# Kernel optimization log

Measured on AMD Instinct MI355X. Metric: run time of the kernel, lower is better.

## Reference

```python
import jax, jax.numpy as jnp
import numpy as np

N, E, B = 50000, 400000, 8
ND, ED, H, L = 32, 16, 128, 3

def setup_inputs() -> dict:
    key = jax.random.key(0)
    ks = jax.random.split(key, 32)
    s = 0.05
    inp = {
        'x': jax.random.normal(ks[0], (N, ND), jnp.float32),
        'edge_attr': jax.random.normal(ks[1], (E, ED), jnp.float32),
        'global_feature': jax.random.normal(ks[2], (B, 1), jnp.float32),
        'edge_index': jax.random.randint(ks[3], (2, E), 0, N, jnp.int64),
        'batch': jnp.sort(jax.random.randint(ks[4], (N,), 0, B, jnp.int64)),
        # embeddings
        'Wn': jax.random.normal(ks[5], (ND, H), jnp.float32) * s,
        'bn': jnp.zeros((H,), jnp.float32),
        'We': jax.random.normal(ks[6], (ED, H), jnp.float32) * s,
        'be': jnp.zeros((H,), jnp.float32),
        'Wg': jax.random.normal(ks[7], (1, H), jnp.float32) * s,
        'bg': jnp.zeros((H,), jnp.float32),
        # message-passing layers (stacked over L)
        'mW1': jax.random.normal(ks[8], (L, 3 * H, H), jnp.float32) * s,
        'mb1': jnp.zeros((L, H), jnp.float32),
        'mW2': jax.random.normal(ks[9], (L, H, H), jnp.float32) * s,
        'mb2': jnp.zeros((L, H), jnp.float32),
        'uW1': jax.random.normal(ks[10], (L, 2 * H, H), jnp.float32) * s,
        'ub1': jnp.zeros((L, H), jnp.float32),
        'uW2': jax.random.normal(ks[11], (L, H, H), jnp.float32) * s,
        'ub2': jnp.zeros((L, H), jnp.float32),
        # readout MLP
        'rW1': jax.random.normal(ks[12], (2 * H, H), jnp.float32) * s,
        'rb1': jnp.zeros((H,), jnp.float32),
        'rW2': jax.random.normal(ks[13], (H, H // 2), jnp.float32) * s,
        'rb2': jnp.zeros((H // 2,), jnp.float32),
        'rW3': jax.random.normal(ks[14], (H // 2, 1), jnp.float32) * s,
        'rb3': jnp.zeros((1,), jnp.float32),
    }
    return inp

def reference(x, edge_attr, global_feature, Wn, bn, We, be, Wg, bg,
              mW1, mb1, mW2, mb2, uW1, ub1, uW2, ub2,
              rW1, rb1, rW2, rb2, rW3, rb3, edge_index, batch):
    h = x @ Wn + bn                      # [N,H]
    e = edge_attr @ We + be              # [E,H]
    g = global_feature @ Wg + bg         # [B,H]
    src, dst = edge_index[0], edge_index[1]  # PyG: x_j=source, x_i=target, aggregate at target
    for l in range(L):
        m_in = jnp.concatenate([h[dst], h[src], e], axis=1)            # [E,3H]
        m = jax.nn.relu(m_in @ mW1[l] + mb1[l]) @ mW2[l] + mb2[l]       # [E,H]
        aggr = jax.ops.segment_sum(m, dst, num_segments=N)              # [N,H]
        u_in = jnp.concatenate([h, aggr], axis=1)                       # [N,2H]
        upd = jax.nn.relu(u_in @ uW1[l] + ub1[l]) @ uW2[l] + ub2[l]
        h = h + upd
    counts = jax.ops.segment_sum(jnp.ones((N,), h.dtype), batch, num_segments=B)
    pooled = jax.ops.segment_sum(h, batch, num_segments=B) / jnp.maximum(counts, 1.0)[:, None]
    final = jnp.concatenate([pooled, g], axis=1)                        # [B,2H]
    out = jax.nn.relu(final @ rW1 + rb1)
    out = jax.nn.relu(out @ rW2 + rb2)
    return out @ rW3 + rb3                                              # [B,1]
```

## Files before the change

### kernel.cpp

```cpp
#include <hip/hip_runtime.h>

#define NN 50000
#define NPAD 50048
#define NE 400000
#define NBATCH 8
#define NDIM 32
#define EDIM 16
#define H 128
#define NLAYERS 3
#define CHUNK_ELEMS 4096
#define NODE_CHUNKS 24
#define ZW_CHUNK 8192
#define NSB 196
#define ZEB 128

#define EMB_B 1563
#define DEG_B 1563
#define ZWB (NLAYERS * 8)
#define WEFB NLAYERS
#define WUB (NLAYERS * 257)
#define P1_B (EMB_B + DEG_B + ZWB + WEFB + WUB)
#define K2_B (NSB + NLAYERS * NODE_CHUNKS)
#define ZDZS_B (NPAD / 64)
#define ZE_B (NE / ZEB)
#define ZZ_B (ZDZS_B + ZE_B)

typedef __attribute__((ext_vector_type(8))) __bf16 bf16x8;
typedef __attribute__((ext_vector_type(16))) float f32x16;
typedef __attribute__((ext_vector_type(8))) short short8;
typedef __attribute__((ext_vector_type(2))) float v2f;

__device__ __forceinline__ void block_sync_lds() {
  asm volatile("s_waitcnt lgkmcnt(0)\ns_barrier" ::: "memory");
}
__device__ __forceinline__ v2f bf2f(unsigned u) {
  v2f r;
  r.x = __uint_as_float(u << 16);
  r.y = __uint_as_float(u & 0xffff0000u);
  return r;
}

__global__ __launch_bounds__(256) void p1_kernel(
    const float* __restrict__ x, const float* __restrict__ Wn,
    const float* __restrict__ bn, __bf16* __restrict__ hb,
    const int* __restrict__ ei, int* __restrict__ deg,
    const float* __restrict__ mW1, __bf16* __restrict__ ZW,
    const float* __restrict__ mb1, const float* __restrict__ We,
    const float* __restrict__ be, __bf16* __restrict__ WefS,
    float* __restrict__ bm, const float* __restrict__ uW1,
    const float* __restrict__ mW2, const float* __restrict__ mb2,
    float* __restrict__ Wu, float* __restrict__ va) {
  __shared__ __align__(16) float smem[NDIM * H + 32 * NDIM];
  int bi = blockIdx.x;
  int tid = threadIdx.x;
  if (bi < EMB_B) {
    float* Ws = smem;
    float* xs = smem + NDIM * H;
    int nbase = bi * 32;
    for (int f = tid; f < NDIM * H; f += 256) Ws[f] = Wn[f];
    for (int f = tid; f < 32 * NDIM; f += 256) {
      int gi = nbase * NDIM + f;
      xs[f] = (gi < NN * NDIM) ? x[gi] : 0.f;
    }
    __syncthreads();
    int j = tid & 127, g = tid >> 7;
    float wcol[NDIM];
#pragma unroll
    for (int k = 0; k < NDIM; ++k) wcol[k] = Ws[k * H + j];
    float b = bn[j];
    for (int nn = 0; nn < 16; ++nn) {
      int node = nbase + g * 16 + nn;
      if (node < NN) {
        float acc = b;
        const float4* xv = (const float4*)&xs[(g * 16 + nn) * NDIM];
#pragma unroll
        for (int k4 = 0; k4 < NDIM / 4; ++k4) {
          float4 v = xv[k4];
          acc = fmaf(v.x, wcol[k4 * 4 + 0], acc);
          acc = fmaf(v.y, wcol[k4 * 4 + 1], acc);
          acc = fmaf(v.z, wcol[k4 * 4 + 2], acc);
          acc = fmaf(v.w, wcol[k4 * 4 + 3], acc);
        }
        hb[(size_t)node * H + j] = (__bf16)acc;
      }
    }
  } else if (bi < EMB_B + DEG_B) {
    int e = (bi - EMB_B) * 256 + tid;
    if (e < NE) atomicAdd(&deg[ei[NE + e]], 1);
  } else if (bi < EMB_B + DEG_B + ZWB) {
    int bb = bi - EMB_B - DEG_B;
    int l = bb / 8;
    int c = bb % 8;
    const float* w1 = mW1 + (size_t)l * 384 * H;
    __bf16* dst = ZW + ((size_t)l * 8 + c) * ZW_CHUNK;
    for (int it = 0; it < 32; it += 4) {
      float wv[4];
#pragma unroll
      for (int q = 0; q < 4; ++q) {
        int flat = (it + q) * 256 + tid;
        int j = flat & 7;
        int lane = (flat >> 3) & 63;
        int nt = (flat >> 9) & 7;
        int k = c * 16 + ((lane >> 5) << 3) + j;
        int n = nt * 32 + (lane & 31);
        wv[q] = (n < 128) ? w1[(size_t)k * H + n]
                          : w1[(size_t)(128 + k) * H + (n - 128)];
      }
#pragma unroll
      for (int q = 0; q < 4; ++q) {
        int flat = (it + q) * 256 + tid;
        int hilo = flat >> 12;
        __bf16 hi = (__bf16)wv[q];
        __bf16 lo = (__bf16)(wv[q] - (float)hi);
        dst[flat] = hilo ? lo : hi;
      }
    }
  } else if (bi < EMB_B + DEG_B + ZWB + WEFB) {
    int l = bi - (EMB_B + DEG_B + ZWB);
    float* WeS = smem;
    float* beS = smem + 2048;
    float* wefT = smem + 2176;
    for (int f = tid; f < EDIM * H; f += 256) WeS[f] = We[f];
    if (tid < 128) beS[tid] = be[tid];
    __syncthreads();
    if (tid < 128) {
      int n = tid;
      const float* w1 = mW1 + (size_t)l * 384 * H + (size_t)256 * H + n;
      float acc[EDIM];
#pragma unroll
      for (int i = 0; i < EDIM; ++i) acc[i] = 0.f;
      float accb = 0.f;
      for (int c = 0; c < H; c += 4) {
        float w0 = w1[(size_t)(c + 0) * H];
        float w1v = w1[(size_t)(c + 1) * H];
        float w2 = w1[(size_t)(c + 2) * H];
        float w3 = w1[(size_t)(c + 3) * H];
        accb = fmaf(beS[c + 0], w0, accb);
        accb = fmaf(beS[c + 1], w1v, accb);
        accb = fmaf(beS[c + 2], w2, accb);
        accb = fmaf(beS[c + 3], w3, accb);
#pragma unroll
        for (int i = 0; i < EDIM; ++i) {
          acc[i] = fmaf(WeS[i * H + c + 0], w0, acc[i]);
          acc[i] = fmaf(WeS[i * H + c + 1], w1v, acc[i]);
          acc[i] = fmaf(WeS[i * H + c + 2], w2, acc[i]);
          acc[i] = fmaf(WeS[i * H + c + 3], w3, acc[i]);
        }
      }
#pragma unroll
      for (int i = 0; i < EDIM; ++i) wefT[i * H + n] = acc[i];
      bm[l * H + n] = mb1[l * H + n] + accb;
    }
    __syncthreads();
    {
      int nt = tid >> 6, lane = tid & 63;
      int n = nt * 32 + (lane & 31);
      int half = lane >> 5;
      __bf16* dst = WefS + (size_t)l * CHUNK_ELEMS;
#pragma unroll
      for (int j = 0; j < 8; ++j) {
        int k = half * 8 + j;
        float w = wefT[k * H + n];
        __bf16 hi = (__bf16)w;
        __bf16 lo = (__bf16)(w - (float)hi);
        dst[((0 * 4 + nt) * 64 + lane) * 8 + j] = hi;
        dst[((1 * 4 + nt) * 64 + lane) * 8 + j] = lo;
      }
    }
  } else {
    int bb = bi - (EMB_B + DEG_B + ZWB + WEFB);
    int l = bb / 257;
    int r = bb % 257;
    int j = tid & 127, hf = tid >> 7;
    const float* u1 = uW1 + (size_t)l * 256 * H;
    if (r < 128) {
      if (tid < 128) Wu[((size_t)l * 256 + r) * H + j] = u1[(size_t)r * H + j];
    } else {
      float* rowS = smem;
      float* redS = smem + 128;
      if (tid < 128)
        rowS[tid] = (r < 256) ? mW2[((size_t)l * H + (r - 128)) * H + tid]
                              : mb2[l * H + tid];
      __syncthreads();
      int cb = hf * 64;
      float s0 = 0.f, s1 = 0.f, s2 = 0.f, s3 = 0.f;
      for (int c = 0; c < 64; c += 4) {
        float a0 = u1[(size_t)(128 + cb + c + 0) * H + j];
        float a1 = u1[(size_t)(128 + cb + c + 1) * H + j];
        float a2 = u1[(size_t)(128 + cb + c + 2) * H + j];
        float a3 = u1[(size_t)(128 + cb + c + 3) * H + j];
        s0 = fmaf(rowS[cb + c + 0], a0, s0);
        s1 = fmaf(rowS[cb + c + 1], a1, s1);
        s2 = fmaf(rowS[cb + c + 2], a2, s2);
        s3 = fmaf(rowS[cb + c + 3], a3, s3);
      }
      float s = (s0 + s1) + (s2 + s3);
      if (hf == 1) redS[j] = s;
      __syncthreads();
      if (hf == 0) {
        float tot = s + redS[j];
        if (r < 256) Wu[((size_t)l * 256 + r) * H + j] = tot;
        else va[l * H + j] = tot;
      }
    }
  }
}

__global__ __launch_bounds__(256) void k2_kernel(
    const int* __restrict__ deg, int* __restrict__ bsum,
    const float* __restrict__ Wu, const float* __restrict__ uW2,
    __bf16* __restrict__ WnS) {
  __shared__ int ws[4];
  int bi = blockIdx.x;
  int tid = threadIdx.x;
  if (bi < NSB) {
    int i = bi * 256 + tid;
    int lane = tid & 63, wid = tid >> 6;
    int v = (i < NN) ? deg[i] : 0;
#pragma unroll
    for (int off = 32; off; off >>= 1) v += __shfl_down(v, off);
    if (lane == 0) ws[wid] = v;
    __syncthreads();
    if (tid == 0) bsum[bi] = ws[0] + ws[1] + ws[2] + ws[3];
  } else {
    int idx = bi - NSB;
    int l = idx / NODE_CHUNKS;
    int c = idx % NODE_CHUNKS;
    int nt = tid >> 6, lane = tid & 63;
    int n = nt * 32 + (lane & 31);
    int half = lane >> 5;
    __bf16* dst = WnS + ((size_t)l * NODE_CHUNKS + c) * CHUNK_ELEMS;
#pragma unroll
    for (int j = 0; j < 8; ++j) {
      float w;
      if (c < 16) {
        int k = c * 16 + half * 8 + j;
        w = Wu[((size_t)l * 256 + k) * H + n];
      } else {
        int k = (c - 16) * 16 + half * 8 + j;
        w = uW2[((size_t)l * H + k) * H + n];
      }
      __bf16 hi = (__bf16)w;
      __bf16 lo = (__bf16)(w - (float)hi);
      dst[((0 * 4 + nt) * 64 + lane) * 8 + j] = hi;
      dst[((1 * 4 + nt) * 64 + lane) * 8 + j] = lo;
    }
  }
}

__global__ __launch_bounds__(256) void scan2_kernel(const int* __restrict__ bsum,
                                                    int* __restrict__ boff) {
  __shared__ int s[256];
  int t = threadIdx.x;
  int v = (t < NSB) ? bsum[t] : 0;
  s[t] = v;
  __syncthreads();
  for (int off = 1; off < 256; off <<= 1) {
    int u = (t >= off) ? s[t - off] : 0;
    __syncthreads();
    s[t] += u;
    __syncthreads();
  }
  if (t < NSB) boff[t] = s[t] - v;
}

__global__ __launch_bounds__(256) void scan3_kernel(const int* __restrict__ deg,
                                                    const int* __restrict__ boff,
                                                    int* __restrict__ cursor) {
  __shared__ int wsum[4], woff[4];
  int i = blockIdx.x * 256 + threadIdx.x;
  int lane = threadIdx.x & 63, wid = threadIdx.x >> 6;
  int orig = (i < NN) ? deg[i] : 0;
  int v = orig;
#pragma unroll
  for (int off = 1; off < 64; off <<= 1) {
    int u = __shfl_up(v, off);
    if (lane >= off) v += u;
  }
  if (lane == 63) wsum[wid] = v;
  __syncthreads();
  if (threadIdx.x == 0) {
    int r = 0;
#pragma unroll
    for (int w = 0; w < 4; ++w) {
      woff[w] = r;
      r += wsum[w];
    }
  }
  __syncthreads();
  if (i < NN) cursor[i] = (v - orig) + woff[wid] + boff[blockIdx.x];
}

__global__ __launch_bounds__(256) void scatter_kernel(
    const int* __restrict__ ei, int* __restrict__ cursor,
    int* __restrict__ srcSrt, const float* __restrict__ ea,
    __bf16* __restrict__ eaSrt) {
  int e = blockIdx.x * 256 + threadIdx.x;
  if (e < NE) {
    int d = ei[NE + e];
    int s = ei[e];
    const float4* ep = (const float4*)(ea + (size_t)e * EDIM);
    float4 v0 = ep[0], v1 = ep[1], v2 = ep[2], v3 = ep[3];
    int pos = atomicAdd(&cursor[d], 1);
    srcSrt[pos] = s;
    union { __bf16 b[16]; uint4 u[2]; } pk;
    pk.b[0] = (__bf16)v0.x;  pk.b[1] = (__bf16)v0.y;
    pk.b[2] = (__bf16)v0.z;  pk.b[3] = (__bf16)v0.w;
    pk.b[4] = (__bf16)v1.x;  pk.b[5] = (__bf16)v1.y;
    pk.b[6] = (__bf16)v1.z;  pk.b[7] = (__bf16)v1.w;
    pk.b[8] = (__bf16)v2.x;  pk.b[9] = (__bf16)v2.y;
    pk.b[10] = (__bf16)v2.z; pk.b[11] = (__bf16)v2.w;
    pk.b[12] = (__bf16)v3.x; pk.b[13] = (__bf16)v3.y;
    pk.b[14] = (__bf16)v3.z; pk.b[15] = (__bf16)v3.w;
    uint4* op = (uint4*)(eaSrt + (size_t)pos * EDIM);
    op[0] = pk.u[0];
    op[1] = pk.u[1];
  }
}

__global__ __launch_bounds__(256) void zz_kernel(
    const __bf16* __restrict__ hb, const __bf16* __restrict__ ZW,
    const float* __restrict__ bm, __bf16* __restrict__ z,
    const __bf16* __restrict__ eaSrt, const __bf16* __restrict__ WefS,
    __bf16* __restrict__ zePre) {
  __shared__ __align__(16) __bf16 Bt[2][ZW_CHUNK];
  int bi = blockIdx.x;
  int tid = threadIdx.x;
  int wid = tid >> 6, lane = tid & 63, m = lane & 31, half = lane >> 5;
  if (bi < ZDZS_B) {
    int rg = wid & 1;
    int nh = wid >> 1;
    int nb = bi * 64;
    int row = nb + rg * 32 + m;
    const __bf16* aH = hb + (size_t)row * H + half * 8;
    const short8* gW = (const short8*)ZW;
    short8* sB0 = (short8*)&Bt[0][0];
    short8* sB1 = (short8*)&Bt[1][0];
#pragma unroll
    for (int q = 0; q < 4; ++q) sB0[tid + q * 256] = gW[tid + q * 256];
    short8 p0 = gW[1024 + tid], p1 = gW[1024 + tid + 256];
    short8 p2 = gW[1024 + tid + 512], p3 = gW[1024 + tid + 768];
    f32x16 acc[4];
#pragma unroll
    for (int ntl = 0; ntl < 4; ++ntl)
#pragma unroll
      for (int r = 0; r < 16; ++r) acc[ntl][r] = 0.f;
    bf16x8 a = *(const bf16x8*)aH;
    block_sync_lds();

    for (int s = 0; s < 8; ++s) {
      int buf = s & 1;
      bf16x8 na = a;
      if (s + 1 < 8) na = *(const bf16x8*)(aH + (s + 1) * 16);
      if (s + 1 < 8) {
        short8* sb = buf ? sB0 : sB1;
        sb[tid] = p0;
        sb[tid + 256] = p1;
        sb[tid + 512] = p2;
        sb[tid + 768] = p3;
        if (s + 2 < 8) {
          p0 = gW[(size_t)(s + 2) * 1024 + tid];
          p1 = gW[(size_t)(s + 2) * 1024 + tid + 256];
          p2 = gW[(size_t)(s + 2) * 1024 + tid + 512];
          p3 = gW[(size_t)(s + 2) * 1024 + tid + 768];
        }
      }
      const __bf16* bb = &Bt[buf][0];
#pragma unroll
      for (int ntl = 0; ntl < 4; ++ntl) {
        int nt = nh * 4 + ntl;
        bf16x8 bh = *(const bf16x8*)&bb[((0 * 8 + nt) * 64 + lane) * 8];
        bf16x8 bl = *(const bf16x8*)&bb[((1 * 8 + nt) * 64 + lane) * 8];
        acc[ntl] = __builtin_amdgcn_mfma_f32_32x32x16_bf16(a, bh, acc[ntl], 0, 0, 0);
        acc[ntl] = __builtin_amdgcn_mfma_f32_32x32x16_bf16(a, bl, acc[ntl], 0, 0, 0);
      }
      a = na;
      if (s + 1 < 8) block_sync_lds();
    }

    float bmv[4];
#pragma unroll
    for (int ntl = 0; ntl < 4; ++ntl) {
      int nt = nh * 4 + ntl;
      bmv[ntl] = (nt < 4) ? bm[nt * 32 + m] : 0.f;
    }
#pragma unroll
    for (int ntl = 0; ntl < 4; ++ntl) {
      int nt = nh * 4 + ntl;
#pragma unroll
      for (int r = 0; r < 16; ++r) {
        int rowi = (r & 3) + 8 * (r >> 2) + 4 * half;
        z[(size_t)(nb + rg * 32 + rowi) * 256 + nt * 32 + m] =
            (__bf16)(acc[ntl][r] + bmv[ntl]);
      }
    }
  } else {
    __bf16* Bf = &Bt[0][0];
    ((short8*)Bf)[tid] = ((const short8*)WefS)[tid];
    ((short8*)Bf)[tid + 256] = ((const short8*)WefS)[tid + 256];
    int ebase = (bi - ZDZS_B) * ZEB + wid * 32;
    bf16x8 a = *(const bf16x8*)(eaSrt + (size_t)(ebase + m) * EDIM + half * 8);
    f32x16 acc[4];
#pragma unroll
    for (int nt = 0; nt < 4; ++nt)
#pragma unroll
      for (int r = 0; r < 16; ++r) acc[nt][r] = 0.f;
    block_sync_lds();
#pragma unroll
    for (int nt = 0; nt < 4; ++nt) {
      bf16x8 bh = *(const bf16x8*)&Bf[((0 * 4 + nt) * 64 + lane) * 8];
      bf16x8 bl = *(const bf16x8*)&Bf[((1 * 4 + nt) * 64 + lane) * 8];
      acc[nt] = __builtin_amdgcn_mfma_f32_32x32x16_bf16(a, bh, acc[nt], 0, 0, 0);
      acc[nt] = __builtin_amdgcn_mfma_f32_32x32x16_bf16(a, bl, acc[nt], 0, 0, 0);
    }
#pragma unroll
    for (int nt = 0; nt < 4; ++nt) {
#pragma unroll
      for (int r = 0; r < 16; ++r) {
        int rowi = (r & 3) + 8 * (r >> 2) + 4 * half;
        zePre[(size_t)(ebase + rowi) * H + nt * 32 + m] = (__bf16)acc[nt][r];
      }
    }
  }
}

__global__ __launch_bounds__(256) void edge_aggr_kernel(
    const __bf16* __restrict__ z, const int* __restrict__ srcSrt,
    const int* __restrict__ cend, const __bf16* __restrict__ zePre,
    __bf16* __restrict__ aggrB) {
  int node = blockIdx.x * 4 + (threadIdx.x >> 6);
  int lane = threadIdx.x & 63;
  int c0 = lane * 2;
  int end = cend[node];
  int start = node ? cend[node - 1] : 0;
  v2f acc = {0.f, 0.f};
  if (start < end) {
    v2f zd = bf2f(*(const unsigned*)(z + (size_t)node * 256 + c0));
    int sArr[4];
#pragma unroll
    for (int p = 0; p < 4; ++p)
      if (start + p < end) sArr[p] = srcSrt[start + p];
    for (int e0 = start; e0 < end; e0 += 4) {
      unsigned zsb[4], zeb[4];
#pragma unroll
      for (int p = 0; p < 4; ++p) {
        if (e0 + p < end) {
          zsb[p] = *(const unsigned*)(z + (size_t)sArr[p] * 256 + 128 + c0);
          zeb[p] = *(const unsigned*)(zePre + (size_t)(e0 + p) * H + c0);
        }
      }
#pragma unroll
      for (int p = 0; p < 4; ++p)
        if (e0 + 4 + p < end) sArr[p] = srcSrt[e0 + 4 + p];
#pragma unroll
      for (int p = 0; p < 4; ++p) {
        if (e0 + p < end) {
          v2f t = zd + bf2f(zsb[p]) + bf2f(zeb[p]);
          acc.x += fmaxf(t.x, 0.f);
          acc.y += fmaxf(t.y, 0.f);
        }
      }
    }
  }
  union { __bf16 b[2]; unsigned u; } pk;
  pk.b[0] = (__bf16)acc.x;
  pk.b[1] = (__bf16)acc.y;
  *(unsigned*)(aggrB + (size_t)node * H + c0) = pk.u;
}

__global__ __launch_bounds__(256) void node_update_mfma_kernel(
    __bf16* __restrict__ hb, const __bf16* __restrict__ aggrB,
    const int* __restrict__ deg, const __bf16* __restrict__ WnS,
    const float* __restrict__ ub1, const float* __restrict__ va,
    const float* __restrict__ ub2) {
  __shared__ __align__(16) __bf16 Bt[2][CHUNK_ELEMS];
  __shared__ __bf16 hid[2][32][132];
  __shared__ float degS[64];
  int tid = threadIdx.x;
  int nb = blockIdx.x * 64;
  if (tid < 64) degS[tid] = (float)deg[nb + tid];
  int wid = tid >> 6, lane = tid & 63, m = lane & 31, half = lane >> 5;
  int rg = wid & 1;
  int nh = wid >> 1;
  int row = nb + rg * 32 + m;
  const __bf16* aHb = hb + (size_t)row * H + half * 8;
  const __bf16* aGb = aggrB + (size_t)row * H + half * 8;
  const short8* gW = (const short8*)WnS;
  short8* sB0 = (short8*)&Bt[0][0];
  short8* sB1 = (short8*)&Bt[1][0];
  sB0[tid] = gW[tid];
  sB0[tid + 256] = gW[tid + 256];
  short8 p0 = gW[512 + tid], p1 = gW[512 + tid + 256];
  float bv1[2], bva[2];
#pragma unroll
  for (int ntl = 0; ntl < 2; ++ntl) {
    int nt = nh * 2 + ntl;
    bv1[ntl] = ub1[nt * 32 + m];
    bva[ntl] = va[nt * 32 + m];
  }
  f32x16 acc[2];
#pragma unroll
  for (int ntl = 0; ntl < 2; ++ntl)
#pragma unroll
    for (int r = 0; r < 16; ++r) acc[ntl][r] = 0.f;
  bf16x8 acur = *(const bf16x8*)aHb;
  block_sync_lds();

  for (int s = 0; s < 16; ++s) {
    int buf = s & 1;
    bf16x8 anext = acur;
    if (s + 1 < 16) {
      int sp = s + 1;
      anext = (sp < 8) ? *(const bf16x8*)(aHb + sp * 16)
                       : *(const bf16x8*)(aGb + (sp - 8) * 16);
    }
    {
      short8* sb = buf ? sB0 : sB1;
      sb[tid] = p0;
      sb[tid + 256] = p1;
      if (s + 2 < NODE_CHUNKS) {
        p0 = gW[(size_t)(s + 2) * 512 + tid];
        p1 = gW[(size_t)(s + 2) * 512 + tid + 256];
      }
    }
    const __bf16* bb = &Bt[buf][0];
#pragma unroll
    for (int ntl = 0; ntl < 2; ++ntl) {
      int nt = nh * 2 + ntl;
      bf16x8 bh = *(const bf16x8*)&bb[((0 * 4 + nt) * 64 + lane) * 8];
      bf16x8 bl = *(const bf16x8*)&bb[((1 * 4 + nt) * 64 + lane) * 8];
      acc[ntl] = __builtin_amdgcn_mfma_f32_32x32x16_bf16(acur, bh, acc[ntl], 0, 0, 0);
      acc[ntl] = __builtin_amdgcn_mfma_f32_32x32x16_bf16(acur, bl, acc[ntl], 0, 0, 0);
    }
    acur = anext;
    block_sync_lds();
  }

#pragma unroll
  for (int ntl = 0; ntl < 2; ++ntl) {
    int nt = nh * 2 + ntl;
#pragma unroll
    for (int r = 0; r < 16; ++r) {
      int rowi = (r & 3) + 8 * (r >> 2) + 4 * half;
      float v = acc[ntl][r] + bv1[ntl] + degS[rg * 32 + rowi] * bva[ntl];
      hid[rg][rowi][nt * 32 + m] = (__bf16)fmaxf(v, 0.f);
      acc[ntl][r] = 0.f;
    }
  }
  block_sync_lds();

  for (int s = 16; s < NODE_CHUNKS; ++s) {
    int buf = s & 1;
    if (s + 1 < NODE_CHUNKS) {
      short8* sb = buf ? sB0 : sB1;
      sb[tid] = p0;
      sb[tid + 256] = p1;
      if (s + 2 < NODE_CHUNKS) {
        p0 = gW[(size_t)(s + 2) * 512 + tid];
        p1 = gW[(size_t)(s + 2) * 512 + tid + 256];
      }
    }
    bf16x8 ah = *(const bf16x8*)&hid[rg][m][(s - 16) * 16 + half * 8];
    const __bf16* bb = &Bt[buf][0];
#pragma unroll
    for (int ntl = 0; ntl < 2; ++ntl) {
      int nt = nh * 2 + ntl;
      bf16x8 bh = *(const bf16x8*)&bb[((0 * 4 + nt) * 64 + lane) * 8];
      bf16x8 bl = *(const bf16x8*)&bb[((1 * 4 + nt) * 64 + lane) * 8];
      acc[ntl] = __builtin_amdgcn_mfma_f32_32x32x16_bf16(ah, bh, acc[ntl], 0, 0, 0);
      acc[ntl] = __builtin_amdgcn_mfma_f32_32x32x16_bf16(ah, bl, acc[ntl], 0, 0, 0);
    }
    if (s + 1 < NODE_CHUNKS) block_sync_lds();
  }

#pragma unroll
  for (int ntl = 0; ntl < 2; ++ntl) {
    int nt = nh * 2 + ntl;
    float b2 = ub2[nt * 32 + m];
#pragma unroll
    for (int r = 0; r < 16; ++r) {
      int rowi = (r & 3) + 8 * (r >> 2) + 4 * half;
      size_t idx = (size_t)(nb + rg * 32 + rowi) * H + nt * 32 + m;
      float hv = (float)hb[idx];
      hb[idx] = (__bf16)(hv + acc[ntl][r] + b2);
    }
  }
}

__global__ __launch_bounds__(256) void pool_kernel(
    const __bf16* __restrict__ hb, const int* __restrict__ batch,
    float* __restrict__ pooled, int* __restrict__ counts) {
  __shared__ float pS[NBATCH * H];
  __shared__ int cS[NBATCH];
  int tid = threadIdx.x;
  for (int i = tid; i < NBATCH * H; i += 256) pS[i] = 0.f;
  if (tid < NBATCH) cS[tid] = 0;
  __syncthreads();
  int c = tid & 15;
  int r0 = tid >> 4;
  int nbase = blockIdx.x * 128;
  v2f acc4[4] = {{0.f, 0.f}, {0.f, 0.f}, {0.f, 0.f}, {0.f, 0.f}};
  int cnt = 0;
  int cur = -1;
#pragma unroll
  for (int i = 0; i < 8; ++i) {
    int n = nbase + i * 16 + r0;
    if (n >= NN) break;
    int b = batch[n];
    if (b != cur) {
      if (cur >= 0) {
#pragma unroll
        for (int q = 0; q < 4; ++q) {
          atomicAdd(&pS[cur * H + c * 8 + q * 2], acc4[q].x);
          atomicAdd(&pS[cur * H + c * 8 + q * 2 + 1], acc4[q].y);
          acc4[q].x = 0.f;
          acc4[q].y = 0.f;
        }
        if (c == 0) atomicAdd(&cS[cur], cnt);
        cnt = 0;
      }
      cur = b;
    }
    uint4 v = *(const uint4*)(hb + (size_t)n * H + c * 8);
    acc4[0] += bf2f(v.x);
    acc4[1] += bf2f(v.y);
    acc4[2] += bf2f(v.z);
    acc4[3] += bf2f(v.w);
    cnt++;
  }
  if (cur >= 0) {
#pragma unroll
    for (int q = 0; q < 4; ++q) {
      atomicAdd(&pS[cur * H + c * 8 + q * 2], acc4[q].x);
      atomicAdd(&pS[cur * H + c * 8 + q * 2 + 1], acc4[q].y);
    }
    if (c == 0) atomicAdd(&cS[cur], cnt);
  }
  __syncthreads();
  for (int i = tid; i < NBATCH * H; i += 256) {
    float v = pS[i];
    if (v != 0.f) unsafeAtomicAdd(&pooled[i], v);
  }
  if (tid < NBATCH) {
    int cv = cS[tid];
    if (cv) atomicAdd(&counts[tid], cv);
  }
}

__global__ __launch_bounds__(128) void readout_kernel(
    const float* __restrict__ pooled, const int* __restrict__ counts,
    const float* __restrict__ gf, const float* __restrict__ Wg,
    const float* __restrict__ bg, const float* __restrict__ rW1,
    const float* __restrict__ rb1, const float* __restrict__ rW2,
    const float* __restrict__ rb2, const float* __restrict__ rW3,
    const float* __restrict__ rb3, float* __restrict__ out) {
  __shared__ float fin[256];
  __shared__ float t1[128];
  __shared__ float t2[64];
  int j = threadIdx.x;
  int b = blockIdx.x;
  float cnt = (float)counts[b];
  if (cnt < 1.f) cnt = 1.f;
  fin[j] = pooled[b * H + j] / cnt;
  fin[H + j] = fmaf(gf[b], Wg[j], bg[j]);
  __syncthreads();
  float a = rb1[j];
  for (int k = 0; k < 256; ++k) a = fmaf(fin[k], rW1[k * H + j], a);
  t1[j] = fmaxf(a, 0.f);
  __syncthreads();
  if (j < 64) {
    float a2 = rb2[j];
    for (int k = 0; k < 128; ++k) a2 = fmaf(t1[k], rW2[k * 64 + j], a2);
    t2[j] = fmaxf(a2, 0.f);
  }
  __syncthreads();
  if (j < 64) {
    float p = t2[j] * rW3[j];
#pragma unroll
    for (int off = 32; off; off >>= 1) p += __shfl_down(p, off);
    if (j == 0) out[b] = p + rb3[0];
  }
}

extern "C" void kernel_launch(void* const* d_in, const int* in_sizes, int n_in,
                              void* d_out, int out_size, void* d_ws, size_t ws_size,
                              hipStream_t stream) {
  const float* x   = (const float*)d_in[0];
  const float* ea  = (const float*)d_in[1];
  const float* gf  = (const float*)d_in[2];
  const int*   ei  = (const int*)d_in[3];
  const int*   bat = (const int*)d_in[4];
  const float* Wn  = (const float*)d_in[5];
  const float* bn  = (const float*)d_in[6];
  const float* We  = (const float*)d_in[7];
  const float* be  = (const float*)d_in[8];
  const float* Wg  = (const float*)d_in[9];
  const float* bg  = (const float*)d_in[10];
  const float* mW1 = (const float*)d_in[11];
  const float* mb1 = (const float*)d_in[12];
  const float* mW2 = (const float*)d_in[13];
  const float* mb2 = (const float*)d_in[14];
  const float* uW1 = (const float*)d_in[15];
  const float* ub1 = (const float*)d_in[16];
  const float* uW2 = (const float*)d_in[17];
  const float* ub2 = (const float*)d_in[18];
  const float* rW1 = (const float*)d_in[19];
  const float* rb1 = (const float*)d_in[20];
  const float* rW2 = (const float*)d_in[21];
  const float* rb2 = (const float*)d_in[22];
  const float* rW3 = (const float*)d_in[23];
  const float* rb3 = (const float*)d_in[24];

  char* p = (char*)d_ws;
  __bf16* hb     = (__bf16*)p; p += (size_t)NPAD * H * 2;
  __bf16* aggrB  = (__bf16*)p; p += (size_t)NPAD * H * 2;
  __bf16* z      = (__bf16*)p; p += (size_t)NPAD * 256 * 2;
  __bf16* zePre  = (__bf16*)p; p += (size_t)NE * H * 2;
  __bf16* eaSrt  = (__bf16*)p; p += (size_t)NE * EDIM * 2;
  int*    srcSrt = (int*)p;    p += (size_t)NE * 4;
  __bf16* ZW     = (__bf16*)p; p += (size_t)NLAYERS * 8 * ZW_CHUNK * 2;
  __bf16* WnS    = (__bf16*)p; p += (size_t)NLAYERS * NODE_CHUNKS * CHUNK_ELEMS * 2;
  __bf16* WefS   = (__bf16*)p; p += (size_t)NLAYERS * CHUNK_ELEMS * 2;
  float*  bm     = (float*)p;  p += (size_t)NLAYERS * H * 4;
  float*  Wu     = (float*)p;  p += (size_t)NLAYERS * 256 * H * 4;
  float*  va     = (float*)p;  p += (size_t)NLAYERS * H * 4;
  int*    deg    = (int*)p;    p += (size_t)NPAD * 4;
  int*    cursor = (int*)p;    p += (size_t)NPAD * 4;
  int*    bsum   = (int*)p;    p += 256 * 4;
  int*    boff   = (int*)p;    p += 256 * 4;
  float*  pooled = (float*)p;  p += (size_t)NBATCH * H * 4;
  int*    counts = (int*)p;    p += 64;

  hipMemsetAsync(deg, 0, (size_t)NPAD * 4, stream);
  hipMemsetAsync(cursor, 0, (size_t)NPAD * 4, stream);
  hipMemsetAsync(pooled, 0, (size_t)NBATCH * H * 4, stream);
  hipMemsetAsync(counts, 0, 64, stream);

  p1_kernel<<<P1_B, 256, 0, stream>>>(x, Wn, bn, hb, ei, deg, mW1, ZW, mb1, We,
                                      be, WefS, bm, uW1, mW2, mb2, Wu, va);
  k2_kernel<<<K2_B, 256, 0, stream>>>(deg, bsum, Wu, uW2, WnS);
  scan2_kernel<<<1, 256, 0, stream>>>(bsum, boff);
  scan3_kernel<<<NSB, 256, 0, stream>>>(deg, boff, cursor);
  scatter_kernel<<<(NE + 255) / 256, 256, 0, stream>>>(ei, cursor, srcSrt, ea,
                                                       eaSrt);

  for (int l = 0; l < NLAYERS; ++l) {
    zz_kernel<<<ZZ_B, 256, 0, stream>>>(
        hb, ZW + (size_t)l * 8 * ZW_CHUNK, bm + (size_t)l * H, z,
        eaSrt, WefS + (size_t)l * CHUNK_ELEMS, zePre);
    edge_aggr_kernel<<<NPAD / 4, 256, 0, stream>>>(
        z, srcSrt, cursor, zePre, aggrB);
    node_update_mfma_kernel<<<NPAD / 64, 256, 0, stream>>>(
        hb, aggrB, deg, WnS + (size_t)l * NODE_CHUNKS * CHUNK_ELEMS,
        ub1 + (size_t)l * H, va + (size_t)l * H, ub2 + (size_t)l * H);
  }

  pool_kernel<<<NPAD / 128, 256, 0, stream>>>(hb, bat, pooled, counts);
  readout_kernel<<<NBATCH, 128, 0, stream>>>(pooled, counts, gf, Wg, bg, rW1,
                                             rb1, rW2, rb2, rW3, rb3,
                                             (float*)d_out);
}
```

Measured before the change: 489.3 us.

## Fuse mean-pooling into final node update, merge scan kernels, deepen edge prefetch

Removes the separate pool kernel by accumulating pooled sums in LDS inside the last layer's node-update kernel, with per-graph counts computed by extra blocks in k2. The two-stage offset scan is merged so each scan block recomputes the block-sum prefix itself, which drops one launch. The edge aggregation loop is widened from 4 to 8 edges in flight to expose more memory-level parallelism. The trade-offs are per-element LDS float atomics in the node kernel (sorted batch ids make these contend on the same addresses), redundant prefix work in every scan block, and higher register use in the aggregation loop.

```diff
diff --git a/kernel.cpp b/kernel.cpp
--- a/kernel.cpp
+++ b/kernel.cpp
@@ -20,7 +20,7 @@
 #define WEFB NLAYERS
 #define WUB (NLAYERS * 257)
 #define P1_B (EMB_B + DEG_B + ZWB + WEFB + WUB)
-#define K2_B (NSB + NLAYERS * NODE_CHUNKS)
+#define K2_B (NSB + NLAYERS * NODE_CHUNKS + NSB)
 #define ZDZS_B (NPAD / 64)
 #define ZE_B (NE / ZEB)
 #define ZZ_B (ZDZS_B + ZE_B)
@@ -209,7 +209,8 @@
 __global__ __launch_bounds__(256) void k2_kernel(
     const int* __restrict__ deg, int* __restrict__ bsum,
     const float* __restrict__ Wu, const float* __restrict__ uW2,
-    __bf16* __restrict__ WnS) {
+    __bf16* __restrict__ WnS, const int* __restrict__ batch,
+    int* __restrict__ counts) {
   __shared__ int ws[4];
   int bi = blockIdx.x;
   int tid = threadIdx.x;
@@ -222,7 +223,7 @@
     if (lane == 0) ws[wid] = v;
     __syncthreads();
     if (tid == 0) bsum[bi] = ws[0] + ws[1] + ws[2] + ws[3];
-  } else {
+  } else if (bi < NSB + NLAYERS * NODE_CHUNKS) {
     int idx = bi - NSB;
     int l = idx / NODE_CHUNKS;
     int c = idx % NODE_CHUNKS;
@@ -245,15 +246,20 @@
       dst[((0 * 4 + nt) * 64 + lane) * 8 + j] = hi;
       dst[((1 * 4 + nt) * 64 + lane) * 8 + j] = lo;
     }
-  }
-}
-
-__global__ __launch_bounds__(256) void scan2_kernel(const int* __restrict__ bsum,
-                                                    int* __restrict__ boff) {
+  } else {
+    int i = (bi - NSB - NLAYERS * NODE_CHUNKS) * 256 + tid;
+    if (i < NN) atomicAdd(&counts[batch[i]], 1);
+  }
+}
+
+__global__ __launch_bounds__(256) void scan3_kernel(const int* __restrict__ deg,
+                                                    const int* __restrict__ bsum,
+                                                    int* __restrict__ cursor) {
   __shared__ int s[256];
+  __shared__ int wsum[4], woff[4];
   int t = threadIdx.x;
-  int v = (t < NSB) ? bsum[t] : 0;
-  s[t] = v;
+  int bv = (t < NSB) ? bsum[t] : 0;
+  s[t] = bv;
   __syncthreads();
   for (int off = 1; off < 256; off <<= 1) {
     int u = (t >= off) ? s[t - off] : 0;
@@ -261,15 +267,11 @@
     s[t] += u;
     __syncthreads();
   }
-  if (t < NSB) boff[t] = s[t] - v;
-}
-
-__global__ __launch_bounds__(256) void scan3_kernel(const int* __restrict__ deg,
-                                                    const int* __restrict__ boff,
-                                                    int* __restrict__ cursor) {
-  __shared__ int wsum[4], woff[4];
-  int i = blockIdx.x * 256 + threadIdx.x;
-  int lane = threadIdx.x & 63, wid = threadIdx.x >> 6;
+  int boff_b = s[blockIdx.x] - bsum[blockIdx.x];
+  __syncthreads();
+
+  int i = blockIdx.x * 256 + t;
+  int lane = t & 63, wid = t >> 6;
   int orig = (i < NN) ? deg[i] : 0;
   int v = orig;
 #pragma unroll
@@ -279,7 +281,7 @@
   }
   if (lane == 63) wsum[wid] = v;
   __syncthreads();
-  if (threadIdx.x == 0) {
+  if (t == 0) {
     int r = 0;
 #pragma unroll
     for (int w = 0; w < 4; ++w) {
@@ -288,7 +290,7 @@
     }
   }
   __syncthreads();
-  if (i < NN) cursor[i] = (v - orig) + woff[wid] + boff[blockIdx.x];
+  if (i < NN) cursor[i] = (v - orig) + woff[wid] + boff_b;
 }
 
 __global__ __launch_bounds__(256) void scatter_kernel(
@@ -436,24 +438,24 @@
   v2f acc = {0.f, 0.f};
   if (start < end) {
     v2f zd = bf2f(*(const unsigned*)(z + (size_t)node * 256 + c0));
-    int sArr[4];
-#pragma unroll
-    for (int p = 0; p < 4; ++p)
+    int sArr[8];
+#pragma unroll
+    for (int p = 0; p < 8; ++p)
       if (start + p < end) sArr[p] = srcSrt[start + p];
-    for (int e0 = start; e0 < end; e0 += 4) {
-      unsigned zsb[4], zeb[4];
-#pragma unroll
-      for (int p = 0; p < 4; ++p) {
+    for (int e0 = start; e0 < end; e0 += 8) {
+      unsigned zsb[8], zeb[8];
+#pragma unroll
+      for (int p = 0; p < 8; ++p) {
         if (e0 + p < end) {
           zsb[p] = *(const unsigned*)(z + (size_t)sArr[p] * 256 + 128 + c0);
           zeb[p] = *(const unsigned*)(zePre + (size_t)(e0 + p) * H + c0);
         }
       }
 #pragma unroll
-      for (int p = 0; p < 4; ++p)
-        if (e0 + 4 + p < end) sArr[p] = srcSrt[e0 + 4 + p];
-#pragma unroll
-      for (int p = 0; p < 4; ++p) {
+      for (int p = 0; p < 8; ++p)
+        if (e0 + 8 + p < end) sArr[p] = srcSrt[e0 + 8 + p];
+#pragma unroll
+      for (int p = 0; p < 8; ++p) {
         if (e0 + p < end) {
           v2f t = zd + bf2f(zsb[p]) + bf2f(zeb[p]);
           acc.x += fmaxf(t.x, 0.f);
@@ -472,7 +474,8 @@
     __bf16* __restrict__ hb, const __bf16* __restrict__ aggrB,
     const int* __restrict__ deg, const __bf16* __restrict__ WnS,
     const float* __restrict__ ub1, const float* __restrict__ va,
-    const float* __restrict__ ub2) {
+    const float* __restrict__ ub2, const int* __restrict__ batch,
+    float* __restrict__ pooled, int doPool) {
   __shared__ __align__(16) __bf16 Bt[2][CHUNK_ELEMS];
   __shared__ __bf16 hid[2][32][132];
   __shared__ float degS[64];
@@ -573,6 +576,15 @@
     if (s + 1 < NODE_CHUNKS) block_sync_lds();
   }
 
+  float* pS = (float*)&Bt[0][0];
+  int* bS = (int*)&hid[0][0][0];
+  if (doPool) {
+    block_sync_lds();
+    if (tid < 64) bS[tid] = (nb + tid < NN) ? batch[nb + tid] : -1;
+    for (int i = tid; i < NBATCH * H; i += 256) pS[i] = 0.f;
+    block_sync_lds();
+  }
+
 #pragma unroll
   for (int ntl = 0; ntl < 2; ++ntl) {
     int nt = nh * 2 + ntl;
@@ -580,70 +592,27 @@
 #pragma unroll
     for (int r = 0; r < 16; ++r) {
       int rowi = (r & 3) + 8 * (r >> 2) + 4 * half;
-      size_t idx = (size_t)(nb + rg * 32 + rowi) * H + nt * 32 + m;
+      int lr2 = rg * 32 + rowi;
+      size_t idx = (size_t)(nb + lr2) * H + nt * 32 + m;
       float hv = (float)hb[idx];
-      hb[idx] = (__bf16)(hv + acc[ntl][r] + b2);
-    }
-  }
-}
-
-__global__ __launch_bounds__(256) void pool_kernel(
-    const __bf16* __restrict__ hb, const int* __restrict__ batch,
-    float* __restrict__ pooled, int* __restrict__ counts) {
-  __shared__ float pS[NBATCH * H];
-  __shared__ int cS[NBATCH];
-  int tid = threadIdx.x;
-  for (int i = tid; i < NBATCH * H; i += 256) pS[i] = 0.f;
-  if (tid < NBATCH) cS[tid] = 0;
-  __syncthreads();
-  int c = tid & 15;
-  int r0 = tid >> 4;
-  int nbase = blockIdx.x * 128;
-  v2f acc4[4] = {{0.f, 0.f}, {0.f, 0.f}, {0.f, 0.f}, {0.f, 0.f}};
-  int cnt = 0;
-  int cur = -1;
-#pragma unroll
-  for (int i = 0; i < 8; ++i) {
-    int n = nbase + i * 16 + r0;
-    if (n >= NN) break;
-    int b = batch[n];
-    if (b != cur) {
-      if (cur >= 0) {
-#pragma unroll
-        for (int q = 0; q < 4; ++q) {
-          atomicAdd(&pS[cur * H + c * 8 + q * 2], acc4[q].x);
-          atomicAdd(&pS[cur * H + c * 8 + q * 2 + 1], acc4[q].y);
-          acc4[q].x = 0.f;
-          acc4[q].y = 0.f;
+      float val = hv + acc[ntl][r] + b2;
+      hb[idx] = (__bf16)val;
+      if (doPool) {
+        int b = bS[lr2];
+        if (b >= 0) {
+          float pv = (float)(__bf16)val;
+          atomicAdd(&pS[b * H + nt * 32 + m], pv);
         }
-        if (c == 0) atomicAdd(&cS[cur], cnt);
-        cnt = 0;
-      }
-      cur = b;
-    }
-    uint4 v = *(const uint4*)(hb + (size_t)n * H + c * 8);
-    acc4[0] += bf2f(v.x);
-    acc4[1] += bf2f(v.y);
-    acc4[2] += bf2f(v.z);
-    acc4[3] += bf2f(v.w);
-    cnt++;
-  }
-  if (cur >= 0) {
-#pragma unroll
-    for (int q = 0; q < 4; ++q) {
-      atomicAdd(&pS[cur * H + c * 8 + q * 2], acc4[q].x);
-      atomicAdd(&pS[cur * H + c * 8 + q * 2 + 1], acc4[q].y);
-    }
-    if (c == 0) atomicAdd(&cS[cur], cnt);
-  }
-  __syncthreads();
-  for (int i = tid; i < NBATCH * H; i += 256) {
-    float v = pS[i];
-    if (v != 0.f) unsafeAtomicAdd(&pooled[i], v);
-  }
-  if (tid < NBATCH) {
-    int cv = cS[tid];
-    if (cv) atomicAdd(&counts[tid], cv);
+      }
+    }
+  }
+
+  if (doPool) {
+    block_sync_lds();
+    for (int i = tid; i < NBATCH * H; i += 256) {
+      float v = pS[i];
+      if (v != 0.f) unsafeAtomicAdd(&pooled[i], v);
+    }
   }
 }
 
@@ -727,7 +696,6 @@
   int*    deg    = (int*)p;    p += (size_t)NPAD * 4;
   int*    cursor = (int*)p;    p += (size_t)NPAD * 4;
   int*    bsum   = (int*)p;    p += 256 * 4;
-  int*    boff   = (int*)p;    p += 256 * 4;
   float*  pooled = (float*)p;  p += (size_t)NBATCH * H * 4;
   int*    counts = (int*)p;    p += 64;
 
@@ -738,9 +706,8 @@
 
   p1_kernel<<<P1_B, 256, 0, stream>>>(x, Wn, bn, hb, ei, deg, mW1, ZW, mb1, We,
                                       be, WefS, bm, uW1, mW2, mb2, Wu, va);
-  k2_kernel<<<K2_B, 256, 0, stream>>>(deg, bsum, Wu, uW2, WnS);
-  scan2_kernel<<<1, 256, 0, stream>>>(bsum, boff);
-  scan3_kernel<<<NSB, 256, 0, stream>>>(deg, boff, cursor);
+  k2_kernel<<<K2_B, 256, 0, stream>>>(deg, bsum, Wu, uW2, WnS, bat, counts);
+  scan3_kernel<<<NSB, 256, 0, stream>>>(deg, bsum, cursor);
   scatter_kernel<<<(NE + 255) / 256, 256, 0, stream>>>(ei, cursor, srcSrt, ea,
                                                        eaSrt);
 
@@ -752,10 +719,10 @@
         z, srcSrt, cursor, zePre, aggrB);
     node_update_mfma_kernel<<<NPAD / 64, 256, 0, stream>>>(
         hb, aggrB, deg, WnS + (size_t)l * NODE_CHUNKS * CHUNK_ELEMS,
-        ub1 + (size_t)l * H, va + (size_t)l * H, ub2 + (size_t)l * H);
-  }
-
-  pool_kernel<<<NPAD / 128, 256, 0, stream>>>(hb, bat, pooled, counts);
+        ub1 + (size_t)l * H, va + (size_t)l * H, ub2 + (size_t)l * H,
+        bat, pooled, (l == NLAYERS - 1) ? 1 : 0);
+  }
+
   readout_kernel<<<NBATCH, 128, 0, stream>>>(pooled, counts, gf, Wg, bg, rW1,
                                              rb1, rW2, rb2, rW3, rb3,
                                              (float*)d_out);
```

After: 1.076 ms. 120% more time.
